# Kernel optimization log

Measured on AMD Instinct MI355X. Metric: run time of the kernel, lower is better.

Reference implementation:

```python
import jax, jax.numpy as jnp
import numpy as np

E, D, H, T = 8, 1024, 2048, 2048  # num_expert, d_model, d_hidden, tokens

def setup_inputs() -> dict:
    key = jax.random.key(0)
    ks = jax.random.split(key, 7)
    return {
        "moe_inp": jax.random.normal(ks[0], (T, D), jnp.float32),
        "Wg": jax.random.normal(ks[1], (D, E), jnp.float32) * 0.02,
        "bg": jnp.zeros((E,), jnp.float32),
        "W1": jax.random.normal(ks[2], (E, D, H), jnp.float32) * 0.02,
        "b1": jnp.zeros((E, H), jnp.float32),
        "W2": jax.random.normal(ks[3], (E, H, D), jnp.float32) * 0.02,
        "b2": jnp.zeros((E, D), jnp.float32),
        "top_k": 2,
    }

def reference(moe_inp, Wg, bg, W1, b1, W2, b2, top_k):
    # NaiveGate: linear gate, top-k select, softmax over the selected logits
    logits = moe_inp @ Wg + bg                      # [T, E]
    top_vals, top_idx = jax.lax.top_k(logits, top_k)  # [T, k]
    gate_score = jax.nn.softmax(top_vals, axis=-1)    # [T, k]

    # Exact (no capacity drop) MoE: scan over experts, mask-combine.
    # Equivalent math to scatter -> per-expert FFN -> gather -> bmm(gate_score, ...).
    def body(acc, xs):
        e, w1, bb1, w2, bb2 = xs
        h = jax.nn.gelu(moe_inp @ w1 + bb1)          # [T, H]
        y = h @ w2 + bb2                             # [T, D]
        w = jnp.sum(jnp.where(top_idx == e, gate_score, 0.0), axis=-1)  # [T]
        return acc + w[:, None] * y, None

    init = jnp.zeros_like(moe_inp)
    xs = (jnp.arange(E), W1, b1, W2, b2)
    moe_outp, _ = jax.lax.scan(body, init, xs)
    return moe_outp, top_idx
```

## Files before the change

kernel.cpp:

```cpp
#include <hip/hip_runtime.h>
#include <stdint.h>

#define T_TOK 2048
#define D_DIM 1024
#define H_DIM 2048
#define N_EXP 8
#define MAXS  5120

#define WS_CNT    0
#define WS_POFF   64
#define WS_BTOK   256
#define WS_BW     (WS_BTOK + N_EXP*2048*4)
#define WS_XG     (WS_BW + N_EXP*2048*4)
#define WS_HBUF   (WS_XG + (size_t)MAXS*1024*2)
#define WS_W1T    (WS_HBUF + (size_t)MAXS*2048*2)
#define WS_W2T    (WS_W1T + (size_t)N_EXP*1024*2048*2)

typedef __bf16 bf16x8 __attribute__((ext_vector_type(8)));
typedef float  f32x4  __attribute__((ext_vector_type(4)));

__device__ __forceinline__ unsigned short f2bf(float f) {
  unsigned int u = __float_as_uint(f);
  u += 0x7fffu + ((u >> 16) & 1u);
  return (unsigned short)(u >> 16);
}

__device__ __forceinline__ float gelu_tanh(float x) {
  float u = 0.7978845608028654f * (x + 0.044715f * x * x * x);
  return 0.5f * x * (1.0f + tanhf(u));
}

__global__ void zero_kernel(float4* __restrict__ out4, int* __restrict__ cnt) {
  int i = blockIdx.x * 256 + threadIdx.x;
  out4[i] = make_float4(0.f, 0.f, 0.f, 0.f);
  if (blockIdx.x == 0 && threadIdx.x < N_EXP) cnt[threadIdx.x] = 0;
}

__global__ void gate_kernel(const float* __restrict__ x, const float* __restrict__ Wg,
                            const float* __restrict__ bg, float* __restrict__ out_idx,
                            int* __restrict__ cnt, int* __restrict__ btok,
                            float* __restrict__ bw) {
  const int lane = threadIdx.x & 63;
  const int t = blockIdx.x * 4 + (threadIdx.x >> 6);
  float p[8];
#pragma unroll
  for (int i = 0; i < 8; ++i) p[i] = 0.f;
  const float* xr = x + (size_t)t * D_DIM;
  for (int i = lane; i < D_DIM; i += 64) {
    const float xv = xr[i];
    const float4 wa = ((const float4*)(Wg + i * 8))[0];
    const float4 wb = ((const float4*)(Wg + i * 8))[1];
    p[0] += xv * wa.x; p[1] += xv * wa.y; p[2] += xv * wa.z; p[3] += xv * wa.w;
    p[4] += xv * wb.x; p[5] += xv * wb.y; p[6] += xv * wb.z; p[7] += xv * wb.w;
  }
#pragma unroll
  for (int off = 32; off > 0; off >>= 1) {
#pragma unroll
    for (int i = 0; i < 8; ++i) p[i] += __shfl_xor(p[i], off);
  }
  if (lane == 0) {
#pragma unroll
    for (int i = 0; i < 8; ++i) p[i] += bg[i];
    int i0 = 0; float v0 = p[0];
#pragma unroll
    for (int i = 1; i < 8; ++i) if (p[i] > v0) { v0 = p[i]; i0 = i; }
    int i1 = -1; float v1 = -3.4e38f;
#pragma unroll
    for (int i = 0; i < 8; ++i) if (i != i0 && p[i] > v1) { v1 = p[i]; i1 = i; }
    const float ex = expf(v1 - v0);
    const float inv = 1.f / (1.f + ex);
    out_idx[t * 2 + 0] = (float)i0;
    out_idx[t * 2 + 1] = (float)i1;
    int s0 = atomicAdd(&cnt[i0], 1);
    btok[i0 * 2048 + s0] = t; bw[i0 * 2048 + s0] = inv;
    int s1 = atomicAdd(&cnt[i1], 1);
    btok[i1 * 2048 + s1] = t; bw[i1 * 2048 + s1] = ex * inv;
  }
}

__global__ void header_kernel(const int* __restrict__ cnt, int* __restrict__ poff) {
  if (threadIdx.x == 0) {
    int off = 0;
    for (int e = 0; e < N_EXP; ++e) { poff[e] = off; off += ((cnt[e] + 127) >> 7) << 7; }
    poff[N_EXP] = off;
  }
}

__global__ void transpose_cvt(const float* __restrict__ in, unsigned short* __restrict__ out,
                              int R, int C) {
  __shared__ float tile[64][65];
  const size_t eo = (size_t)blockIdx.z * R * C;
  const int c0 = blockIdx.x * 64;
  const int r0 = blockIdx.y * 64;
  for (int i = threadIdx.x; i < 4096; i += 256) {
    const int r = i >> 6, c = i & 63;
    tile[r][c] = in[eo + (size_t)(r0 + r) * C + (c0 + c)];
  }
  __syncthreads();
  for (int i = threadIdx.x; i < 4096; i += 256) {
    const int cc = i >> 6, rr = i & 63;
    out[eo + (size_t)(c0 + cc) * R + (r0 + rr)] = f2bf(tile[rr][cc]);
  }
}

__global__ void gather_cvt(const float* __restrict__ x, const int* __restrict__ poff,
                           const int* __restrict__ cnt, const int* __restrict__ btok,
                           unsigned short* __restrict__ Xg) {
  const int s = blockIdx.x;
  if (s >= poff[N_EXP]) return;
  int e = 0;
#pragma unroll
  for (int i = 0; i < N_EXP; ++i) if (s >= poff[i + 1]) e = i + 1;
  const int local = s - poff[e];
  uint2* orow = (uint2*)(Xg + (size_t)s * D_DIM);
  if (local < cnt[e]) {
    const int t = btok[e * 2048 + local];
    const float4 v = ((const float4*)(x + (size_t)t * D_DIM))[threadIdx.x];
    uint2 u;
    u.x = (unsigned)f2bf(v.x) | ((unsigned)f2bf(v.y) << 16);
    u.y = (unsigned)f2bf(v.z) | ((unsigned)f2bf(v.w) << 16);
    orow[threadIdx.x] = u;
  } else {
    orow[threadIdx.x] = make_uint2(0u, 0u);
  }
}

template <int MODE>
__global__ void __launch_bounds__(256) moe_gemm(
    const unsigned short* __restrict__ A, const unsigned short* __restrict__ B,
    const float* __restrict__ bias, const int* __restrict__ poff,
    const int* __restrict__ cnt, const int* __restrict__ btok,
    const float* __restrict__ bw, unsigned short* __restrict__ Hout,
    float* __restrict__ out) {
  constexpr int K = (MODE == 0) ? D_DIM : H_DIM;

  const int e = blockIdx.y >> 4;
  const int mt = blockIdx.y & 15;
  const int base = poff[e];
  const int pcnt = poff[e + 1] - base;
  if (mt * 128 >= pcnt) return;
  const int row0 = base + mt * 128;
  const int n0 = blockIdx.x * 128;

  __shared__ __align__(16) unsigned short As[128 * 32];
  __shared__ __align__(16) unsigned short Bs[128 * 32];

  const int tid = threadIdx.x;
  const int lane = tid & 63;
  const int wv = tid >> 6;
  const int wm = wv >> 1;
  const int wn = wv & 1;

  const unsigned short* Ab = A + (size_t)row0 * K;
  const unsigned short* Bb = B + (size_t)e * ((size_t)H_DIM * D_DIM) + (size_t)n0 * K;

  f32x4 acc[4][4];
#pragma unroll
  for (int i = 0; i < 4; ++i)
#pragma unroll
    for (int j = 0; j < 4; ++j) acc[i][j] = (f32x4)(0.0f);

  const int subr = lane >> 2;
  const int ks = (lane & 3) * 8;
  const int fr = lane & 15;
  const int kq = (lane >> 4) * 8;

  for (int kt = 0; kt < K / 32; ++kt) {
    const int k0 = kt * 32;
#pragma unroll
    for (int it = 0; it < 2; ++it) {
      const int ci = wv + it * 4;
      const int r = ci * 16 + subr;
      const unsigned short* ga = Ab + (size_t)r * K + (k0 + ks);
      const unsigned short* gb = Bb + (size_t)r * K + (k0 + ks);
      __builtin_amdgcn_global_load_lds(
          (__attribute__((address_space(1))) void*)ga,
          (__attribute__((address_space(3))) void*)(As + ci * 16 * 32), 16, 0, 0);
      __builtin_amdgcn_global_load_lds(
          (__attribute__((address_space(1))) void*)gb,
          (__attribute__((address_space(3))) void*)(Bs + ci * 16 * 32), 16, 0, 0);
    }
    __syncthreads();
    bf16x8 av[4], bv[4];
#pragma unroll
    for (int mi = 0; mi < 4; ++mi)
      av[mi] = *(const bf16x8*)(As + (wm * 64 + mi * 16 + fr) * 32 + kq);
#pragma unroll
    for (int ni = 0; ni < 4; ++ni)
      bv[ni] = *(const bf16x8*)(Bs + (wn * 64 + ni * 16 + fr) * 32 + kq);
#pragma unroll
    for (int mi = 0; mi < 4; ++mi)
#pragma unroll
      for (int ni = 0; ni < 4; ++ni)
        acc[mi][ni] = __builtin_amdgcn_mfma_f32_16x16x32_bf16(av[mi], bv[ni], acc[mi][ni], 0, 0, 0);
    __syncthreads();
  }

  if (MODE == 0) {
    const float* bb = bias + (size_t)e * H_DIM + n0;
#pragma unroll
    for (int mi = 0; mi < 4; ++mi) {
      const int rb = wm * 64 + mi * 16 + (lane >> 4) * 4;
#pragma unroll
      for (int r = 0; r < 4; ++r) {
        unsigned short* hp = Hout + (size_t)(row0 + rb + r) * H_DIM + n0;
#pragma unroll
        for (int ni = 0; ni < 4; ++ni) {
          const int col = wn * 64 + ni * 16 + fr;
          hp[col] = f2bf(gelu_tanh(acc[mi][ni][r] + bb[col]));
        }
      }
    }
  } else {
    const float* bb = bias + (size_t)e * D_DIM + n0;
    const int ce = cnt[e];
#pragma unroll
    for (int mi = 0; mi < 4; ++mi) {
      const int rb = wm * 64 + mi * 16 + (lane >> 4) * 4;
#pragma unroll
      for (int r = 0; r < 4; ++r) {
        const int local = mt * 128 + rb + r;
        if (local < ce) {
          const int tok = btok[e * 2048 + local];
          const float w = bw[e * 2048 + local];
          float* op = out + (size_t)tok * D_DIM + n0;
#pragma unroll
          for (int ni = 0; ni < 4; ++ni) {
            const int col = wn * 64 + ni * 16 + fr;
            atomicAdd(op + col, w * (acc[mi][ni][r] + bb[col]));
          }
        }
      }
    }
  }
}

extern "C" void kernel_launch(void* const* d_in, const int* in_sizes, int n_in,
                              void* d_out, int out_size, void* d_ws, size_t ws_size,
                              hipStream_t stream) {
  const float* moe_inp = (const float*)d_in[0];
  const float* Wg = (const float*)d_in[1];
  const float* bg = (const float*)d_in[2];
  const float* W1 = (const float*)d_in[3];
  const float* b1 = (const float*)d_in[4];
  const float* W2 = (const float*)d_in[5];
  const float* b2 = (const float*)d_in[6];
  float* out = (float*)d_out;

  char* ws = (char*)d_ws;
  int* cnt  = (int*)(ws + WS_CNT);
  int* poff = (int*)(ws + WS_POFF);
  int* btok = (int*)(ws + WS_BTOK);
  float* bw = (float*)(ws + WS_BW);
  unsigned short* Xg   = (unsigned short*)(ws + WS_XG);
  unsigned short* Hbuf = (unsigned short*)(ws + WS_HBUF);
  unsigned short* W1t  = (unsigned short*)(ws + WS_W1T);
  unsigned short* W2t  = (unsigned short*)(ws + WS_W2T);

  zero_kernel<<<dim3(2048), dim3(256), 0, stream>>>((float4*)out, cnt);
  gate_kernel<<<dim3(T_TOK / 4), dim3(256), 0, stream>>>(moe_inp, Wg, bg,
                                                         out + (size_t)T_TOK * D_DIM,
                                                         cnt, btok, bw);
  header_kernel<<<dim3(1), dim3(64), 0, stream>>>(cnt, poff);
  transpose_cvt<<<dim3(H_DIM / 64, D_DIM / 64, N_EXP), dim3(256), 0, stream>>>(W1, W1t, D_DIM, H_DIM);
  transpose_cvt<<<dim3(D_DIM / 64, H_DIM / 64, N_EXP), dim3(256), 0, stream>>>(W2, W2t, H_DIM, D_DIM);
  gather_cvt<<<dim3(MAXS), dim3(256), 0, stream>>>(moe_inp, poff, cnt, btok, Xg);
  moe_gemm<0><<<dim3(H_DIM / 128, N_EXP * 16), dim3(256), 0, stream>>>(
      Xg, W1t, b1, poff, cnt, btok, bw, Hbuf, nullptr);
  moe_gemm<1><<<dim3(D_DIM / 128, N_EXP * 16), dim3(256), 0, stream>>>(
      Hbuf, W2t, b2, poff, cnt, btok, bw, nullptr, out);
}
```

Measured before the change: 366.8 us.

## Double-buffer MoE GEMM, split-K second GEMM, remap grid, vectorize weight transpose

```diff
diff --git a/kernel.cpp b/kernel.cpp
--- a/kernel.cpp
+++ b/kernel.cpp
@@ -86,20 +86,39 @@
   }
 }
 
-__global__ void transpose_cvt(const float* __restrict__ in, unsigned short* __restrict__ out,
-                              int R, int C) {
-  __shared__ float tile[64][65];
-  const size_t eo = (size_t)blockIdx.z * R * C;
-  const int c0 = blockIdx.x * 64;
-  const int r0 = blockIdx.y * 64;
-  for (int i = threadIdx.x; i < 4096; i += 256) {
-    const int r = i >> 6, c = i & 63;
-    tile[r][c] = in[eo + (size_t)(r0 + r) * C + (c0 + c)];
+__global__ void transpose_cvt(const float* __restrict__ W1, unsigned short* __restrict__ W1t,
+                              const float* __restrict__ W2, unsigned short* __restrict__ W2t) {
+  const int set = blockIdx.z;
+  const int e = blockIdx.y;
+  const int lin = blockIdx.x;
+  const int R = set ? H_DIM : D_DIM;
+  const int C = set ? D_DIM : H_DIM;
+  const int tx = set ? (lin & 15) : (lin & 31);
+  const int ty = set ? (lin >> 4) : (lin >> 5);
+  const float* in = (set ? W2 : W1) + (size_t)e * (D_DIM * H_DIM);
+  unsigned short* out = (set ? W2t : W1t) + (size_t)e * (D_DIM * H_DIM);
+  const int c0 = tx * 64, r0 = ty * 64;
+  __shared__ float tile[64][68];
+  const int tid = threadIdx.x;
+#pragma unroll
+  for (int p = 0; p < 4; ++p) {
+    const int idx = p * 256 + tid;
+    const int r = idx >> 4, c4 = idx & 15;
+    *(float4*)&tile[r][c4 * 4] = *(const float4*)(in + (size_t)(r0 + r) * C + c0 + c4 * 4);
   }
   __syncthreads();
-  for (int i = threadIdx.x; i < 4096; i += 256) {
-    const int cc = i >> 6, rr = i & 63;
-    out[eo + (size_t)(c0 + cc) * R + (r0 + rr)] = f2bf(tile[rr][cc]);
+#pragma unroll
+  for (int p = 0; p < 2; ++p) {
+    const int idx = p * 256 + tid;
+    const int oc = idx >> 3, seg = idx & 7;
+    unsigned u[4];
+#pragma unroll
+    for (int j = 0; j < 4; ++j) {
+      const unsigned lo = f2bf(tile[seg * 8 + 2 * j][oc]);
+      const unsigned hi = f2bf(tile[seg * 8 + 2 * j + 1][oc]);
+      u[j] = lo | (hi << 16);
+    }
+    *(uint4*)(out + (size_t)(c0 + oc) * R + r0 + seg * 8) = make_uint4(u[0], u[1], u[2], u[3]);
   }
 }
 
@@ -132,18 +151,29 @@
     const int* __restrict__ cnt, const int* __restrict__ btok,
     const float* __restrict__ bw, unsigned short* __restrict__ Hout,
     float* __restrict__ out) {
-  constexpr int K = (MODE == 0) ? D_DIM : H_DIM;
-
-  const int e = blockIdx.y >> 4;
-  const int mt = blockIdx.y & 15;
+  constexpr int K   = (MODE == 0) ? D_DIM : H_DIM;
+  constexpr int NT  = (MODE == 0) ? H_DIM / 128 : D_DIM / 128;
+  constexpr int SK  = (MODE == 0) ? 1 : 2;
+  constexpr int KS  = K / SK;
+  constexpr int NIT = KS / 32;
+
+  const int lin  = blockIdx.x;
+  const int glo  = lin & 7;
+  const int mt   = (lin >> 3) & 15;
+  const int g    = ((lin >> 7) << 3) | glo;
+  const int nt   = g % NT;
+  const int rest = g / NT;
+  const int e    = rest & 7;
+  const int ksl  = rest >> 3;
+
   const int base = poff[e];
   const int pcnt = poff[e + 1] - base;
   if (mt * 128 >= pcnt) return;
   const int row0 = base + mt * 128;
-  const int n0 = blockIdx.x * 128;
-
-  __shared__ __align__(16) unsigned short As[128 * 32];
-  __shared__ __align__(16) unsigned short Bs[128 * 32];
+  const int n0 = nt * 128;
+
+  __shared__ __align__(16) unsigned short As[2][128 * 32];
+  __shared__ __align__(16) unsigned short Bs[2][128 * 32];
 
   const int tid = threadIdx.x;
   const int lane = tid & 63;
@@ -151,8 +181,8 @@
   const int wm = wv >> 1;
   const int wn = wv & 1;
 
-  const unsigned short* Ab = A + (size_t)row0 * K;
-  const unsigned short* Bb = B + (size_t)e * ((size_t)H_DIM * D_DIM) + (size_t)n0 * K;
+  const unsigned short* Ab = A + (size_t)row0 * K + ksl * KS;
+  const unsigned short* Bb = B + (size_t)e * ((size_t)H_DIM * D_DIM) + (size_t)n0 * K + ksl * KS;
 
   f32x4 acc[4][4];
 #pragma unroll
@@ -165,7 +195,7 @@
   const int fr = lane & 15;
   const int kq = (lane >> 4) * 8;
 
-  for (int kt = 0; kt < K / 32; ++kt) {
+  auto stage = [&](int kt, int b) {
     const int k0 = kt * 32;
 #pragma unroll
     for (int it = 0; it < 2; ++it) {
@@ -175,25 +205,30 @@
       const unsigned short* gb = Bb + (size_t)r * K + (k0 + ks);
       __builtin_amdgcn_global_load_lds(
           (__attribute__((address_space(1))) void*)ga,
-          (__attribute__((address_space(3))) void*)(As + ci * 16 * 32), 16, 0, 0);
+          (__attribute__((address_space(3))) void*)(As[b] + ci * 16 * 32), 16, 0, 0);
       __builtin_amdgcn_global_load_lds(
           (__attribute__((address_space(1))) void*)gb,
-          (__attribute__((address_space(3))) void*)(Bs + ci * 16 * 32), 16, 0, 0);
+          (__attribute__((address_space(3))) void*)(Bs[b] + ci * 16 * 32), 16, 0, 0);
     }
+  };
+
+  stage(0, 0);
+  for (int i = 0; i < NIT; ++i) {
+    const int b = i & 1;
     __syncthreads();
+    if (i + 1 < NIT) stage(i + 1, b ^ 1);
     bf16x8 av[4], bv[4];
 #pragma unroll
     for (int mi = 0; mi < 4; ++mi)
-      av[mi] = *(const bf16x8*)(As + (wm * 64 + mi * 16 + fr) * 32 + kq);
+      av[mi] = *(const bf16x8*)(As[b] + (wm * 64 + mi * 16 + fr) * 32 + kq);
 #pragma unroll
     for (int ni = 0; ni < 4; ++ni)
-      bv[ni] = *(const bf16x8*)(Bs + (wn * 64 + ni * 16 + fr) * 32 + kq);
+      bv[ni] = *(const bf16x8*)(Bs[b] + (wn * 64 + ni * 16 + fr) * 32 + kq);
 #pragma unroll
     for (int mi = 0; mi < 4; ++mi)
 #pragma unroll
       for (int ni = 0; ni < 4; ++ni)
         acc[mi][ni] = __builtin_amdgcn_mfma_f32_16x16x32_bf16(av[mi], bv[ni], acc[mi][ni], 0, 0, 0);
-    __syncthreads();
   }
 
   if (MODE == 0) {
@@ -227,7 +262,8 @@
 #pragma unroll
           for (int ni = 0; ni < 4; ++ni) {
             const int col = wn * 64 + ni * 16 + fr;
-            atomicAdd(op + col, w * (acc[mi][ni][r] + bb[col]));
+            const float bias_once = (ksl == 0) ? bb[col] : 0.f;
+            atomicAdd(op + col, w * (acc[mi][ni][r] + bias_once));
           }
         }
       }
@@ -262,11 +298,10 @@
                                                          out + (size_t)T_TOK * D_DIM,
                                                          cnt, btok, bw);
   header_kernel<<<dim3(1), dim3(64), 0, stream>>>(cnt, poff);
-  transpose_cvt<<<dim3(H_DIM / 64, D_DIM / 64, N_EXP), dim3(256), 0, stream>>>(W1, W1t, D_DIM, H_DIM);
-  transpose_cvt<<<dim3(D_DIM / 64, H_DIM / 64, N_EXP), dim3(256), 0, stream>>>(W2, W2t, H_DIM, D_DIM);
+  transpose_cvt<<<dim3(512, N_EXP, 2), dim3(256), 0, stream>>>(W1, W1t, W2, W2t);
   gather_cvt<<<dim3(MAXS), dim3(256), 0, stream>>>(moe_inp, poff, cnt, btok, Xg);
-  moe_gemm<0><<<dim3(H_DIM / 128, N_EXP * 16), dim3(256), 0, stream>>>(
+  moe_gemm<0><<<dim3(2048), dim3(256), 0, stream>>>(
       Xg, W1t, b1, poff, cnt, btok, bw, Hbuf, nullptr);
-  moe_gemm<1><<<dim3(D_DIM / 128, N_EXP * 16), dim3(256), 0, stream>>>(
+  moe_gemm<1><<<dim3(2048), dim3(256), 0, stream>>>(
       Hbuf, W2t, b2, poff, cnt, btok, bw, nullptr, out);
 }
```

Result: faster. 348.8 us (-4.9%).
